# Optimization experiments

Hardware: AMD Instinct MI355X
Metric: run time of the kernel (lower is better)

Reference implementation:

```python
import jax, jax.numpy as jnp
import numpy as np

C = 128        # channels
NHEADS = 8
B = 16
HW = 128       # image side; must satisfy HW*HW == C**2 for the module's final view


def setup_inputs() -> dict:
    key = jax.random.key(0)
    k0, k1, k2, k3, k4 = jax.random.split(key, 5)
    x = jax.random.normal(k0, (B, C, HW, HW), jnp.float32)
    w_qkv = jax.random.normal(k1, (3 * C, C), jnp.float32) * 0.02  # 1x1 conv == dense over channel dim
    b_qkv = jax.random.normal(k2, (3 * C,), jnp.float32) * 0.02
    w_out = jax.random.normal(k3, (C, C), jnp.float32) * 0.02
    b_out = jax.random.normal(k4, (C,), jnp.float32) * 0.02
    return {"x": x, "w_qkv": w_qkv, "b_qkv": b_qkv, "w_out": w_out, "b_out": b_out}


def reference(x, w_qkv, b_qkv, w_out, b_out):
    Bx, Cx, Hs, Ws = x.shape
    d = Cx // NHEADS
    N = Hs * Ws  # flattened spatial tokens
    # QKV 1x1 conv (bias=True)
    qkv = jnp.einsum('oc,bchw->bohw', w_qkv, x) + b_qkv[None, :, None, None]
    q, k, v = jnp.split(qkv, 3, axis=1)          # each (B, C, H, W)
    q = q.reshape(Bx, NHEADS, d, N)
    k = k.reshape(Bx, NHEADS, d, N)
    v = v.reshape(Bx, NHEADS, d, N)
    # scaled dot-product attention over the head-channel dim (d x d scores)
    scores = jnp.einsum('bhdn,bhen->bhde', q, k) / jnp.sqrt(jnp.float32(Cx))
    attn = jax.nn.softmax(scores, axis=-1)
    out = jnp.einsum('bhde,bhen->bhdn', attn, v)  # (B, H, d, N)
    side = N // Cx  # module reshapes to (B, C, N//C, N//C); valid since N == C^2
    out = out.reshape(Bx, Cx, side, side)
    # output 1x1 conv
    return jnp.einsum('oc,bchw->bohw', w_out, out) + b_out[None, :, None, None]
```

## Files before the change

kernel.cpp:

```cpp
#include <hip/hip_runtime.h>
#include <math.h>

#define BB 16
#define CC 128
#define NN 16384
#define NHEADS 8
#define HD 16
#define SCALE 0.08838834764831843f

typedef __attribute__((ext_vector_type(8))) short short8;
typedef __attribute__((ext_vector_type(4))) unsigned short ushort4v;
typedef __attribute__((ext_vector_type(16))) float f32x16;

__global__ __launch_bounds__(256) void k1_gram(const float* __restrict__ x,
                                               float* __restrict__ pG,
                                               float* __restrict__ pS,
                                               int CH) {
    const int chunk = blockIdx.x;
    const int b = blockIdx.y;
    const int tid = threadIdx.x;
    const int w = tid >> 6;
    const int l = tid & 63;
    const int ch0 = tid >> 4;
    const int t4 = tid & 15;
    const int NCB = NN / CH;
    const int NSTAGE = NCB >> 6;

    __shared__ unsigned short lds[2][2][128 * 64];

    const float* xg = x + (size_t)b * CC * NN + (size_t)chunk * NCB;

    f32x16 acc[10];
#pragma unroll
    for (int t = 0; t < 10; ++t)
#pragma unroll
        for (int r = 0; r < 16; ++r) acc[t][r] = 0.0f;

    float csum[8];
#pragma unroll
    for (int k = 0; k < 8; ++k) csum[k] = 0.0f;

    float4 ld[8];

    auto LOAD = [&](int s) {
#pragma unroll
        for (int k = 0; k < 8; ++k)
            ld[k] = *(const float4*)(xg + (size_t)(ch0 + 16 * k) * NN + s * 64 + t4 * 4);
    };

#define CVT(comp, hh, ll)                                                    \
    {                                                                        \
        unsigned int u = __float_as_uint(comp);                              \
        unsigned int r = (u + 0x7fffu + ((u >> 16) & 1u)) >> 16;             \
        float lf = (comp) - __uint_as_float(r << 16);                        \
        hh = (unsigned short)r;                                              \
        ll = (unsigned short)(__float_as_uint(lf) >> 16);                    \
    }

    auto CVW = [&](int buf) {
#pragma unroll
        for (int k = 0; k < 8; ++k) {
            float4 v = ld[k];
            csum[k] += v.x + v.y + v.z + v.w;
            const int ch = ch0 + 16 * k;
            const int idx = ((ch << 6) + (t4 << 2)) ^ ((ch & 7) << 3);
            unsigned short h0, h1, h2, h3, l0, l1, l2, l3;
            CVT(v.x, h0, l0)
            CVT(v.y, h1, l1)
            CVT(v.z, h2, l2)
            CVT(v.w, h3, l3)
            ushort4v hv = {h0, h1, h2, h3};
            ushort4v lv = {l0, l1, l2, l3};
            *(ushort4v*)&lds[buf][0][idx] = hv;
            *(ushort4v*)&lds[buf][1][idx] = lv;
        }
    };

    const int lr = l & 31, lh = l >> 5;

    LOAD(0);
    CVW(0);
    __syncthreads();

    for (int s = 0; s < NSTAGE; ++s) {
        const int bsel = s & 1;
        if (s + 1 < NSTAGE) LOAD(s + 1);

        short8 fh[4], fl[4];
        const int tb = w * 16 + lh * 8;
#pragma unroll
        for (int cb = 0; cb < 4; ++cb) {
            const int ch = cb * 32 + lr;
            const int idx = ((ch << 6) + tb) ^ ((ch & 7) << 3);
            fh[cb] = *(const short8*)&lds[bsel][0][idx];
            fl[cb] = *(const short8*)&lds[bsel][1][idx];
        }

#define TILE(t, bi, bj)                                                                      \
        acc[t] = __builtin_amdgcn_mfma_f32_32x32x16_bf16(fh[bi], fh[bj], acc[t], 0, 0, 0);   \
        acc[t] = __builtin_amdgcn_mfma_f32_32x32x16_bf16(fh[bi], fl[bj], acc[t], 0, 0, 0);   \
        acc[t] = __builtin_amdgcn_mfma_f32_32x32x16_bf16(fl[bi], fh[bj], acc[t], 0, 0, 0);   \
        acc[t] = __builtin_amdgcn_mfma_f32_32x32x16_bf16(fl[bi], fl[bj], acc[t], 0, 0, 0);
        TILE(0, 0, 0) TILE(1, 0, 1) TILE(2, 0, 2) TILE(3, 0, 3) TILE(4, 1, 1)
        TILE(5, 1, 2) TILE(6, 1, 3) TILE(7, 2, 2) TILE(8, 2, 3) TILE(9, 3, 3)
#undef TILE

        if (s + 1 < NSTAGE) CVW((s + 1) & 1);
        __syncthreads();
    }

    float* scr = (float*)&lds[0][0][0];
#pragma unroll
    for (int k = 0; k < 8; ++k) scr[(ch0 + 16 * k) * 16 + t4] = csum[k];
    __syncthreads();
    if (tid < 128) {
        float s2 = 0.0f;
#pragma unroll
        for (int i = 0; i < 16; ++i) s2 += scr[tid * 16 + i];
        pS[(size_t)(b * CH + chunk) * 128 + tid] = s2;
    }
    __syncthreads();

    float* outp = pG + (size_t)(b * CH + chunk) * 10240;
#pragma unroll
    for (int half = 0; half < 2; ++half) {
        if (w > 0) {
#pragma unroll
            for (int tt = 0; tt < 5; ++tt)
#pragma unroll
                for (int r = 0; r < 16; ++r)
                    scr[((w - 1) * 5 + tt) * 1024 + r * 64 + l] = acc[half * 5 + tt][r];
        }
        __syncthreads();
        if (w == 0) {
#pragma unroll
            for (int tt = 0; tt < 5; ++tt)
#pragma unroll
                for (int r = 0; r < 16; ++r)
                    outp[(half * 5 + tt) * 1024 + r * 64 + l] =
                        acc[half * 5 + tt][r]
                        + scr[(0 * 5 + tt) * 1024 + r * 64 + l]
                        + scr[(1 * 5 + tt) * 1024 + r * 64 + l]
                        + scr[(2 * 5 + tt) * 1024 + r * 64 + l];
        }
        __syncthreads();
    }
}

__global__ __launch_bounds__(256) void k1_reduce(const float* __restrict__ pG,
                                                 const float* __restrict__ pS,
                                                 float* __restrict__ G,
                                                 float* __restrict__ sB,
                                                 int CH) {
    const int sg = blockIdx.x;
    const int b = blockIdx.y;
    const int tid = threadIdx.x;

    if (sg < 40) {
        const int e = sg * 256 + tid;
        const int t = e >> 10;
        const int rl = e & 1023;
        float sum = 0.0f;
        const float* p = pG + (size_t)b * CH * 10240 + e;
        for (int ch = 0; ch < CH; ++ch) sum += p[(size_t)ch * 10240];

        int bi, bj;
        if (t < 4)      { bi = 0; bj = t; }
        else if (t < 7) { bi = 1; bj = t - 3; }
        else if (t < 9) { bi = 2; bj = t - 5; }
        else            { bi = 3; bj = 3; }

        const int reg = rl >> 6, lane = rl & 63;
        const int col = bj * 32 + (lane & 31);
        const int row = bi * 32 + (reg & 3) + 8 * (reg >> 2) + 4 * (lane >> 5);
        G[((size_t)b << 14) + row * CC + col] = sum;
        if (bi != bj) G[((size_t)b << 14) + col * CC + row] = sum;
    } else {
        if (tid < 128) {
            float s2 = 0.0f;
            for (int ch = 0; ch < CH; ++ch) s2 += pS[(size_t)(b * CH + ch) * 128 + tid];
            sB[b * CC + tid] = s2;
        }
    }
}

__global__ __launch_bounds__(256) void k2a_attn(const float* __restrict__ G,
                                                const float* __restrict__ sB,
                                                const float* __restrict__ w_qkv,
                                                const float* __restrict__ b_qkv,
                                                float* __restrict__ attn,
                                                float* __restrict__ cpre) {
    const int h = blockIdx.x;
    const int b = blockIdx.y;
    const int tid = threadIdx.x;

    __shared__ float wq_s[HD][132], wk_s[HD][132], Tq[HD][132];
    __shared__ float qs[HD], ks[HD], bqv[HD], bkv[HD], bvv[HD];
    __shared__ float sc[HD][HD + 1];

    for (int idx = tid; idx < HD * CC; idx += 256) {
        int r = idx >> 7, c = idx & 127;
        wq_s[r][c] = w_qkv[(h * HD + r) * CC + c];
        wk_s[r][c] = w_qkv[(CC + h * HD + r) * CC + c];
    }
    if (tid < HD) {
        bqv[tid] = b_qkv[h * HD + tid];
        bkv[tid] = b_qkv[CC + h * HD + tid];
        bvv[tid] = b_qkv[2 * CC + h * HD + tid];
    }
    __syncthreads();

    if (tid < 32) {
        int i = tid & 15;
        bool isK = tid >= 16;
        float sum = 0.0f;
        for (int c = 0; c < CC; ++c)
            sum += (isK ? wk_s[i][c] : wq_s[i][c]) * sB[b * CC + c];
        if (isK) ks[i] = sum; else qs[i] = sum;
    }

    {
        const int c2 = tid & 127;
        const int dh = tid >> 7;
        float t[8];
#pragma unroll
        for (int j = 0; j < 8; ++j) t[j] = 0.0f;
        const float* Gb = G + ((size_t)b << 14);
        for (int c1 = 0; c1 < CC; ++c1) {
            float g = Gb[c1 * CC + c2];
#pragma unroll
            for (int j = 0; j < 8; ++j) t[j] += wq_s[dh * 8 + j][c1] * g;
        }
        __syncthreads();
#pragma unroll
        for (int j = 0; j < 8; ++j) Tq[dh * 8 + j][c2] = t[j];
    }
    __syncthreads();

    {
        const int dd = tid >> 4, e = tid & 15;
        float sum = 0.0f;
        for (int c2 = 0; c2 < CC; ++c2) sum += Tq[dd][c2] * wk_s[e][c2];
        sum += qs[dd] * bkv[e] + bqv[dd] * ks[e] + (float)NN * bqv[dd] * bkv[e];
        sc[dd][e] = sum * SCALE;
    }
    __syncthreads();

    if (tid < HD) {
        const int dd = tid;
        float mx = -1e30f;
#pragma unroll
        for (int e = 0; e < HD; ++e) mx = fmaxf(mx, sc[dd][e]);
        float ex[HD];
        float den = 0.0f;
#pragma unroll
        for (int e = 0; e < HD; ++e) { ex[e] = __expf(sc[dd][e] - mx); den += ex[e]; }
        float inv = 1.0f / den;
        float cp = 0.0f;
#pragma unroll
        for (int e = 0; e < HD; ++e) {
            float a = ex[e] * inv;
            attn[((size_t)b * NHEADS + h) * HD * HD + dd * HD + e] = a;
            cp += a * bvv[e];
        }
        cpre[b * CC + h * HD + dd] = cp;
    }
}

__global__ __launch_bounds__(256) void k2b_M(const float* __restrict__ attn,
                                             const float* __restrict__ cpre,
                                             const float* __restrict__ w_qkv,
                                             const float* __restrict__ w_out,
                                             const float* __restrict__ b_out,
                                             float* __restrict__ Mt,
                                             float* __restrict__ cvec) {
    const int og = blockIdx.x;
    const int b = blockIdx.y;
    const int tid = threadIdx.x;

    __shared__ float Ph[HD][132];
    __shared__ float wo_s[32][129];
    __shared__ float attn_s[CC][HD];
    __shared__ float cpre_s[CC];

    for (int idx = tid; idx < CC * HD; idx += 256)
        attn_s[idx >> 4][idx & 15] = attn[(size_t)b * CC * HD + idx];
    for (int idx = tid; idx < 32 * CC; idx += 256)
        wo_s[idx >> 7][idx & 127] = w_out[(og * 32 + (idx >> 7)) * CC + (idx & 127)];
    if (tid < CC) cpre_s[tid] = cpre[b * CC + tid];
    __syncthreads();

    const int c = tid & 127;
    const int oh = tid >> 7;
    float m[16];
#pragma unroll
    for (int j = 0; j < 16; ++j) m[j] = 0.0f;

    for (int hh = 0; hh < NHEADS; ++hh) {
        for (int idx = tid; idx < HD * CC; idx += 256) {
            int dd = idx >> 7, cc = idx & 127;
            float s = 0.0f;
#pragma unroll
            for (int e = 0; e < HD; ++e)
                s += attn_s[hh * HD + dd][e] * w_qkv[(2 * CC + hh * HD + e) * CC + cc];
            Ph[dd][cc] = s;
        }
        __syncthreads();
#pragma unroll
        for (int dd = 0; dd < HD; ++dd) {
            float p = Ph[dd][c];
#pragma unroll
            for (int j = 0; j < 16; ++j)
                m[j] += wo_s[oh * 16 + j][hh * HD + dd] * p;
        }
        __syncthreads();
    }

    float* mt = Mt + ((size_t)b << 14) + c * CC + og * 32 + oh * 16;
#pragma unroll
    for (int j = 0; j < 16; ++j) mt[j] = m[j];

    if (tid < 32) {
        float s = 0.0f;
        for (int r = 0; r < CC; ++r) s += wo_s[tid][r] * cpre_s[r];
        cvec[b * CC + og * 32 + tid] = s + b_out[og * 32 + tid];
    }
}

__global__ __launch_bounds__(256) void k3_out(const float* __restrict__ x,
                                              const float* __restrict__ Mt,
                                              const float* __restrict__ cvec,
                                              float* __restrict__ y) {
    const int chunk = blockIdx.x;
    const int rh = blockIdx.y;
    const int b = blockIdx.z;
    const int tid = threadIdx.x;

    __shared__ float Mts[CC][68];
    __shared__ float cs[64];

    for (int idx = tid; idx < CC * 64; idx += 256) {
        int o = idx & 63, c = idx >> 6;
        Mts[c][o] = Mt[((size_t)b << 14) + c * CC + rh * 64 + o];
    }
    if (tid < 64) cs[tid] = cvec[b * CC + rh * 64 + tid];
    __syncthreads();

    const int rg = tid >> 5;
    const float* xb = x + (size_t)b * CC * NN + chunk * 256 + (tid & 31) * 8;

    float acc[8][8];
#pragma unroll
    for (int u = 0; u < 8; ++u)
#pragma unroll
        for (int w = 0; w < 8; ++w) acc[u][w] = 0.0f;

    for (int c = 0; c < CC; ++c) {
        float4 xa = *(const float4*)&xb[(size_t)c * NN];
        float4 xc4 = *(const float4*)&xb[(size_t)c * NN + 4];
        float4 m0 = *(const float4*)&Mts[c][rg * 8];
        float4 m1 = *(const float4*)&Mts[c][rg * 8 + 4];
        float mr[8] = {m0.x, m0.y, m0.z, m0.w, m1.x, m1.y, m1.z, m1.w};
        float xv[8] = {xa.x, xa.y, xa.z, xa.w, xc4.x, xc4.y, xc4.z, xc4.w};
#pragma unroll
        for (int u = 0; u < 8; ++u)
#pragma unroll
            for (int w = 0; w < 8; ++w) acc[u][w] += mr[u] * xv[w];
    }

    float* yb = y + (size_t)b * CC * NN + (size_t)(rh * 64 + rg * 8) * NN + chunk * 256 + (tid & 31) * 8;
#pragma unroll
    for (int u = 0; u < 8; ++u) {
        float cadd = cs[rg * 8 + u];
        float4 o0 = {acc[u][0] + cadd, acc[u][1] + cadd, acc[u][2] + cadd, acc[u][3] + cadd};
        float4 o1 = {acc[u][4] + cadd, acc[u][5] + cadd, acc[u][6] + cadd, acc[u][7] + cadd};
        *(float4*)&yb[(size_t)u * NN] = o0;
        *(float4*)&yb[(size_t)u * NN + 4] = o1;
    }
}

extern "C" void kernel_launch(void* const* d_in, const int* in_sizes, int n_in,
                              void* d_out, int out_size, void* d_ws, size_t ws_size,
                              hipStream_t stream) {
    const float* x     = (const float*)d_in[0];
    const float* w_qkv = (const float*)d_in[1];
    const float* b_qkv = (const float*)d_in[2];
    const float* w_out = (const float*)d_in[3];
    const float* b_out = (const float*)d_in[4];
    float* y = (float*)d_out;

    const size_t szG = (size_t)BB * CC * CC;
    const size_t szS = (size_t)BB * CC;
    const size_t szAttn = (size_t)BB * NHEADS * HD * HD;
    const size_t tail = szG + szS + szAttn + szS + szG + szS;

    int CH = 32;
    while (CH > 1 &&
           ((size_t)CH * BB * 10240 + (size_t)CH * BB * CC + tail) * sizeof(float) > ws_size)
        CH >>= 1;

    float* pG   = (float*)d_ws;
    float* pS   = pG + (size_t)CH * BB * 10240;
    float* G    = pS + (size_t)CH * BB * CC;
    float* sB   = G + szG;
    float* attn = sB + szS;
    float* cpre = attn + szAttn;
    float* Mt   = cpre + szS;
    float* cvec = Mt + szG;

    k1_gram<<<dim3(CH, BB), 256, 0, stream>>>(x, pG, pS, CH);
    k1_reduce<<<dim3(41, BB), 256, 0, stream>>>(pG, pS, G, sB, CH);
    k2a_attn<<<dim3(NHEADS, BB), 256, 0, stream>>>(G, sB, w_qkv, b_qkv, attn, cpre);
    k2b_M<<<dim3(4, BB), 256, 0, stream>>>(attn, cpre, w_qkv, w_out, b_out, Mt, cvec);
    k3_out<<<dim3(64, 2, BB), 256, 0, stream>>>(x, Mt, cvec, y);
}
```

Baseline: 418.9 us.

## Move output projection to split-bf16 MFMA and drop low×low Gram term

The final output kernel k3_out is rewritten from scalar FP32 FMAs to 32x32x16 bf16 MFMA. Both the folded matrix M and x are split into hi/lo bf16 halves and combined with three MFMAs, which emulates FP32 precision. k2b_M now writes M as transposed hi/lo bf16 arrays. The Gram kernel drops its lo×lo MFMA term and replaces round-to-nearest with truncation when splitting. This cuts matrix-core work, but the small loss of precision could matter for accuracy, and the output stores are now scattered scalar writes.

Measured after the change: 347.5 us. 1.21x faster.

```diff
diff --git a/kernel.cpp b/kernel.cpp
--- a/kernel.cpp
+++ b/kernel.cpp
@@ -11,6 +11,14 @@
 typedef __attribute__((ext_vector_type(8))) short short8;
 typedef __attribute__((ext_vector_type(4))) unsigned short ushort4v;
 typedef __attribute__((ext_vector_type(16))) float f32x16;
+
+#define CVT(comp, hh, ll)                                                    \
+    {                                                                        \
+        unsigned int u = __float_as_uint(comp);                              \
+        hh = (unsigned short)(u >> 16);                                      \
+        float lf = (comp) - __uint_as_float(u & 0xffff0000u);                \
+        ll = (unsigned short)(__float_as_uint(lf) >> 16);                    \
+    }
 
 __global__ __launch_bounds__(256) void k1_gram(const float* __restrict__ x,
                                                float* __restrict__ pG,
@@ -26,7 +34,7 @@
     const int NCB = NN / CH;
     const int NSTAGE = NCB >> 6;
 
-    __shared__ unsigned short lds[2][2][128 * 64];
+    __shared__ __align__(16) unsigned short lds[2][2][128 * 64];
 
     const float* xg = x + (size_t)b * CC * NN + (size_t)chunk * NCB;
 
@@ -47,15 +55,6 @@
         for (int k = 0; k < 8; ++k)
             ld[k] = *(const float4*)(xg + (size_t)(ch0 + 16 * k) * NN + s * 64 + t4 * 4);
     };
-
-#define CVT(comp, hh, ll)                                                    \
-    {                                                                        \
-        unsigned int u = __float_as_uint(comp);                              \
-        unsigned int r = (u + 0x7fffu + ((u >> 16) & 1u)) >> 16;             \
-        float lf = (comp) - __uint_as_float(r << 16);                        \
-        hh = (unsigned short)r;                                              \
-        ll = (unsigned short)(__float_as_uint(lf) >> 16);                    \
-    }
 
     auto CVW = [&](int buf) {
 #pragma unroll
@@ -99,8 +98,7 @@
 #define TILE(t, bi, bj)                                                                      \
         acc[t] = __builtin_amdgcn_mfma_f32_32x32x16_bf16(fh[bi], fh[bj], acc[t], 0, 0, 0);   \
         acc[t] = __builtin_amdgcn_mfma_f32_32x32x16_bf16(fh[bi], fl[bj], acc[t], 0, 0, 0);   \
-        acc[t] = __builtin_amdgcn_mfma_f32_32x32x16_bf16(fl[bi], fh[bj], acc[t], 0, 0, 0);   \
-        acc[t] = __builtin_amdgcn_mfma_f32_32x32x16_bf16(fl[bi], fl[bj], acc[t], 0, 0, 0);
+        acc[t] = __builtin_amdgcn_mfma_f32_32x32x16_bf16(fl[bi], fh[bj], acc[t], 0, 0, 0);
         TILE(0, 0, 0) TILE(1, 0, 1) TILE(2, 0, 2) TILE(3, 0, 3) TILE(4, 1, 1)
         TILE(5, 1, 2) TILE(6, 1, 3) TILE(7, 2, 2) TILE(8, 2, 3) TILE(9, 3, 3)
 #undef TILE
@@ -272,7 +270,8 @@
                                              const float* __restrict__ w_qkv,
                                              const float* __restrict__ w_out,
                                              const float* __restrict__ b_out,
-                                             float* __restrict__ Mt,
+                                             unsigned short* __restrict__ Mh,
+                                             unsigned short* __restrict__ Ml,
                                              float* __restrict__ cvec) {
     const int og = blockIdx.x;
     const int b = blockIdx.y;
@@ -316,9 +315,14 @@
         __syncthreads();
     }
 
-    float* mt = Mt + ((size_t)b << 14) + c * CC + og * 32 + oh * 16;
-#pragma unroll
-    for (int j = 0; j < 16; ++j) mt[j] = m[j];
+#pragma unroll
+    for (int j = 0; j < 16; ++j) {
+        const int o = og * 32 + oh * 16 + j;
+        unsigned short hh2, ll2;
+        CVT(m[j], hh2, ll2)
+        Mh[((size_t)b << 14) + o * CC + c] = hh2;
+        Ml[((size_t)b << 14) + o * CC + c] = ll2;
+    }
 
     if (tid < 32) {
         float s = 0.0f;
@@ -328,54 +332,108 @@
 }
 
 __global__ __launch_bounds__(256) void k3_out(const float* __restrict__ x,
-                                              const float* __restrict__ Mt,
+                                              const unsigned short* __restrict__ Mh,
+                                              const unsigned short* __restrict__ Ml,
                                               const float* __restrict__ cvec,
                                               float* __restrict__ y) {
     const int chunk = blockIdx.x;
-    const int rh = blockIdx.y;
-    const int b = blockIdx.z;
+    const int b = blockIdx.y;
     const int tid = threadIdx.x;
-
-    __shared__ float Mts[CC][68];
-    __shared__ float cs[64];
-
-    for (int idx = tid; idx < CC * 64; idx += 256) {
-        int o = idx & 63, c = idx >> 6;
-        Mts[c][o] = Mt[((size_t)b << 14) + c * CC + rh * 64 + o];
-    }
-    if (tid < 64) cs[tid] = cvec[b * CC + rh * 64 + tid];
-    __syncthreads();
-
-    const int rg = tid >> 5;
-    const float* xb = x + (size_t)b * CC * NN + chunk * 256 + (tid & 31) * 8;
-
-    float acc[8][8];
-#pragma unroll
-    for (int u = 0; u < 8; ++u)
-#pragma unroll
-        for (int w = 0; w < 8; ++w) acc[u][w] = 0.0f;
-
-    for (int c = 0; c < CC; ++c) {
-        float4 xa = *(const float4*)&xb[(size_t)c * NN];
-        float4 xc4 = *(const float4*)&xb[(size_t)c * NN + 4];
-        float4 m0 = *(const float4*)&Mts[c][rg * 8];
-        float4 m1 = *(const float4*)&Mts[c][rg * 8 + 4];
-        float mr[8] = {m0.x, m0.y, m0.z, m0.w, m1.x, m1.y, m1.z, m1.w};
-        float xv[8] = {xa.x, xa.y, xa.z, xa.w, xc4.x, xc4.y, xc4.z, xc4.w};
-#pragma unroll
-        for (int u = 0; u < 8; ++u)
-#pragma unroll
-            for (int w = 0; w < 8; ++w) acc[u][w] += mr[u] * xv[w];
-    }
-
-    float* yb = y + (size_t)b * CC * NN + (size_t)(rh * 64 + rg * 8) * NN + chunk * 256 + (tid & 31) * 8;
-#pragma unroll
-    for (int u = 0; u < 8; ++u) {
-        float cadd = cs[rg * 8 + u];
-        float4 o0 = {acc[u][0] + cadd, acc[u][1] + cadd, acc[u][2] + cadd, acc[u][3] + cadd};
-        float4 o1 = {acc[u][4] + cadd, acc[u][5] + cadd, acc[u][6] + cadd, acc[u][7] + cadd};
-        *(float4*)&yb[(size_t)u * NN] = o0;
-        *(float4*)&yb[(size_t)u * NN + 4] = o1;
+    const int w = tid >> 6;
+    const int lane = tid & 63;
+
+    __shared__ __align__(16) unsigned short xs[2][2][64 * 128];
+
+    const float* xb = x + (size_t)b * CC * NN + (size_t)chunk * 128;
+
+    short8 Ah[8], Al[8];
+    {
+        const size_t mbase = ((size_t)b << 14) + (size_t)(32 * w + (lane & 31)) * CC;
+#pragma unroll
+        for (int ks = 0; ks < 8; ++ks) {
+            const size_t off = mbase + 16 * ks + 8 * (lane >> 5);
+            Ah[ks] = *(const short8*)&Mh[off];
+            Al[ks] = *(const short8*)&Ml[off];
+        }
+    }
+
+    f32x16 acc[4];
+#pragma unroll
+    for (int t = 0; t < 4; ++t)
+#pragma unroll
+        for (int r = 0; r < 16; ++r) acc[t][r] = 0.0f;
+
+    float ldv[8][4];
+
+    auto LOAD = [&](int s) {
+#pragma unroll
+        for (int k = 0; k < 8; ++k) {
+            const int c0 = w * 4 + k * 16;
+#pragma unroll
+            for (int i = 0; i < 4; ++i)
+                ldv[k][i] = xb[(size_t)(c0 + i) * NN + s * 64 + lane];
+        }
+    };
+
+    auto CVW = [&](int buf) {
+#pragma unroll
+        for (int k = 0; k < 8; ++k) {
+            const int c0 = w * 4 + k * 16;
+            const int idx = lane * 128 + (c0 ^ ((lane & 7) << 3));
+            ushort4v hv, lv;
+#pragma unroll
+            for (int i = 0; i < 4; ++i) {
+                unsigned short hh, ll;
+                CVT(ldv[k][i], hh, ll)
+                hv[i] = hh;
+                lv[i] = ll;
+            }
+            *(ushort4v*)&xs[buf][0][idx] = hv;
+            *(ushort4v*)&xs[buf][1][idx] = lv;
+        }
+    };
+
+    LOAD(0);
+    CVW(0);
+    __syncthreads();
+
+#pragma unroll
+    for (int s = 0; s < 2; ++s) {
+        if (s == 0) LOAD(1);
+#pragma unroll
+        for (int nt = 0; nt < 2; ++nt) {
+            const int nl = nt * 32 + (lane & 31);
+            const int cxor = (nl & 7) << 3;
+            const int rowb = nl * 128;
+#pragma unroll
+            for (int ks = 0; ks < 8; ++ks) {
+                const int idx = rowb + ((16 * ks + 8 * (lane >> 5)) ^ cxor);
+                short8 bh = *(const short8*)&xs[s][0][idx];
+                short8 bl = *(const short8*)&xs[s][1][idx];
+                const int t = s * 2 + nt;
+                acc[t] = __builtin_amdgcn_mfma_f32_32x32x16_bf16(Ah[ks], bh, acc[t], 0, 0, 0);
+                acc[t] = __builtin_amdgcn_mfma_f32_32x32x16_bf16(Ah[ks], bl, acc[t], 0, 0, 0);
+                acc[t] = __builtin_amdgcn_mfma_f32_32x32x16_bf16(Al[ks], bh, acc[t], 0, 0, 0);
+            }
+        }
+        if (s == 0) CVW(1);
+        __syncthreads();
+    }
+
+    float cvv[16];
+#pragma unroll
+    for (int r = 0; r < 16; ++r)
+        cvv[r] = cvec[b * CC + 32 * w + (r & 3) + 8 * (r >> 2) + 4 * (lane >> 5)];
+
+    float* yb = y + (size_t)b * CC * NN + (size_t)chunk * 128;
+#pragma unroll
+    for (int t = 0; t < 4; ++t) {
+        const int n = t * 32 + (lane & 31);
+#pragma unroll
+        for (int r = 0; r < 16; ++r) {
+            const int o = 32 * w + (r & 3) + 8 * (r >> 2) + 4 * (lane >> 5);
+            yb[(size_t)o * NN + n] = acc[t][r] + cvv[r];
+        }
     }
 }
 
@@ -405,12 +463,15 @@
     float* sB   = G + szG;
     float* attn = sB + szS;
     float* cpre = attn + szAttn;
-    float* Mt   = cpre + szS;
-    float* cvec = Mt + szG;
+    float* Mslab = cpre + szS;
+    float* cvec = Mslab + szG;
+
+    unsigned short* Mh = (unsigned short*)Mslab;
+    unsigned short* Ml = Mh + (size_t)BB * CC * CC;
 
     k1_gram<<<dim3(CH, BB), 256, 0, stream>>>(x, pG, pS, CH);
     k1_reduce<<<dim3(41, BB), 256, 0, stream>>>(pG, pS, G, sB, CH);
     k2a_attn<<<dim3(NHEADS, BB), 256, 0, stream>>>(G, sB, w_qkv, b_qkv, attn, cpre);
-    k2b_M<<<dim3(4, BB), 256, 0, stream>>>(attn, cpre, w_qkv, w_out, b_out, Mt, cvec);
-    k3_out<<<dim3(64, 2, BB), 256, 0, stream>>>(x, Mt, cvec, y);
-}
+    k2b_M<<<dim3(4, BB), 256, 0, stream>>>(attn, cpre, w_qkv, w_out, b_out, Mh, Ml, cvec);
+    k3_out<<<dim3(128, BB), 256, 0, stream>>>(x, Mh, Ml, cvec, y);
+}
```
